# Performance work log

Hardware: AMD Instinct MI355X
Metric: run time of the kernel (lower is better)

## Reference

```python
import jax, jax.numpy as jnp
import numpy as np

BS, N, XC, K, YS = 64, 1024, 1024, 256, 768

def setup_inputs() -> dict:
    key = jax.random.key(0)
    ks = jax.random.split(key, 5)
    return {
        "x": jax.random.normal(ks[0], (BS, N, XC), dtype=jnp.float32),
        "y": jax.random.normal(ks[1], (BS, YS), dtype=jnp.float32),
        "W_ch": jax.random.normal(ks[2], (K, XC), dtype=jnp.float32) * 0.02,
        "b_ch": jax.random.normal(ks[3], (K,), dtype=jnp.float32) * 0.02,
        "W_y": jax.random.normal(ks[4], (K, YS), dtype=jnp.float32) * 0.02,
    }

def reference(x, y, W_ch, b_ch, W_y):
    # y_k: [bs, k] (no bias)
    y_k = jnp.einsum('bs,ks->bk', y, W_y)
    # channel affine on every spatial position, batched: [bs, n, k]
    x_k = jnp.einsum('bnc,kc->bnk', x, W_ch) + b_ch
    # add per-sample y_k (broadcast over spatial dim), tanh, softmax over k
    z = jnp.tanh(x_k + y_k[:, None, :])
    attn = jax.nn.softmax(z, axis=-1)
    # torch.cat over dim=0 of per-sample [n, k] blocks -> [bs*n, k]
    return attn.reshape(-1, attn.shape[-1])
```

## Files before the change

kernel.cpp:

```cpp
#include <hip/hip_runtime.h>


#define XC    1024
#define KOUT  256
#define NT    16
#define ZSTR  260
#define ZB    33280
#define LDSZ  34816

typedef float        f32x4_t  __attribute__((ext_vector_type(4)));
typedef unsigned int u32x4_t  __attribute__((ext_vector_type(4)));
typedef unsigned int u32x2_t  __attribute__((ext_vector_type(2)));
typedef __bf16       bf16x8_t __attribute__((ext_vector_type(8)));

__device__ __forceinline__ unsigned short f2bf(float f) {
  unsigned int u = __float_as_uint(f);
  u += 0x7fffu + ((u >> 16) & 1u);
  return (unsigned short)(u >> 16);
}

__device__ __forceinline__ float fast_tanh(float v) {
  float e = __expf(2.0f * v);
  return 1.0f - 2.0f / (e + 1.0f);
}

#define LGKM_BARRIER() do {                                  \
    asm volatile("s_waitcnt lgkmcnt(0)" ::: "memory");       \
    __builtin_amdgcn_s_barrier();                            \
    __builtin_amdgcn_sched_barrier(0);                       \
  } while (0)

__global__ void prep_kernel(const float* __restrict__ Wch,
                            const float* __restrict__ y,
                            const float* __restrict__ Wy,
                            const float* __restrict__ bch,
                            unsigned short* __restrict__ wbf,
                            float* __restrict__ biasws) {
  if (blockIdx.x < 256) {
    const int k = blockIdx.x;
    const int u = threadIdx.x;
    f32x4_t v = ((const f32x4_t*)(Wch + k * XC))[u];
    const int c0   = u << 2;
    const int t    = c0 >> 6;
    const int ch   = (c0 & 63) >> 3;
    const int kk   = ch >> 2;
    const int lg   = ch & 3;
    const int half = (c0 >> 2) & 1;
    const int wv   = k >> 6;
    const int ni   = (k >> 4) & 3;
    const int lr   = k & 15;
    const int lane = (lg << 4) | lr;
    unsigned int lo = (unsigned int)f2bf(v.x) | ((unsigned int)f2bf(v.y) << 16);
    unsigned int hi = (unsigned int)f2bf(v.z) | ((unsigned int)f2bf(v.w) << 16);
    char* p = (char*)wbf +
              ((size_t)((((t << 2) + wv) * 2 + kk) * 4 + ni) << 10) +
              (lane << 4) + (half << 3);
    *(u32x2_t*)p = (u32x2_t){lo, hi};
  } else {
    __shared__ __align__(16) float ys[768];
    const int b = blockIdx.x - 256;
    const int k = threadIdx.x;
    for (int i = k; i < 768; i += 256) ys[i] = y[b * 768 + i];
    __syncthreads();
    const f32x4_t* w4 = (const f32x4_t*)(Wy + k * 768);
    const f32x4_t* y4 = (const f32x4_t*)ys;
    float s = 0.f;
#pragma unroll 8
    for (int i = 0; i < 192; ++i) {
      f32x4_t w = w4[i], a = y4[i];
      s = fmaf(w.x, a.x, s); s = fmaf(w.y, a.y, s);
      s = fmaf(w.z, a.z, s); s = fmaf(w.w, a.w, s);
    }
    biasws[b * 256 + k] = s + bch[k];
  }
}

__global__ __launch_bounds__(256, 4) void fused_kernel(
    const float* __restrict__ x, const unsigned short* __restrict__ wbf,
    const float* __restrict__ bias, float* __restrict__ out) {
  __shared__ __align__(16) unsigned char smem[LDSZ];
  const int tid = threadIdx.x;
  const int l   = tid & 63;
  const int wv  = tid >> 6;
  const int lr  = l & 15;
  const int lg  = l >> 4;
  const int m0  = blockIdx.x << 5;
  const int bidx = m0 >> 10;
  const int rr  = tid >> 4;
  const int c4  = tid & 15;

  f32x4_t acc[2][4];
#pragma unroll
  for (int i = 0; i < 2; ++i)
#pragma unroll
    for (int j = 0; j < 4; ++j) acc[i][j] = (f32x4_t){0.f, 0.f, 0.f, 0.f};

  const float* xb = x + (size_t)m0 * XC + (size_t)rr * XC + (c4 << 2);
  const char* wsrc = (const char*)wbf;
  f32x4_t avA[2], avB[2];
  bf16x8_t bfr[8];

#define LOADA(dst, tt) do {                                                  \
    _Pragma("unroll")                                                        \
    for (int j = 0; j < 2; ++j)                                              \
      dst[j] = *(const f32x4_t*)(xb + (size_t)(j << 4) * XC + ((tt) << 6));  \
  } while (0)

#define LOADB(tt) do {                                                       \
    const char* g = wsrc + (size_t)(tt) * 32768 + (wv << 13) + (l << 4);     \
    _Pragma("unroll")                                                        \
    for (int f = 0; f < 8; ++f)                                              \
      bfr[f] = __builtin_bit_cast(bf16x8_t, *(const u32x4_t*)(g + (f << 10)));\
  } while (0)

#define WRITEA(src, buf) do {                                                \
    _Pragma("unroll")                                                        \
    for (int j = 0; j < 2; ++j) {                                            \
      const int row = (j << 4) + rr;                                         \
      unsigned int lo = (unsigned int)f2bf(src[j].x) |                       \
                        ((unsigned int)f2bf(src[j].y) << 16);                \
      unsigned int hi = (unsigned int)f2bf(src[j].z) |                       \
                        ((unsigned int)f2bf(src[j].w) << 16);                \
      char* p = (char*)smem + ((buf) << 12) + row * 128 +                    \
                (((c4 >> 1) ^ (row & 7)) << 4) + ((c4 & 1) << 3);            \
      *(u32x2_t*)p = (u32x2_t){lo, hi};                                      \
    }                                                                        \
  } while (0)

#define COMPUTE(buf) do {                                                    \
    const u32x4_t* aB = (const u32x4_t*)(smem + ((buf) << 12));              \
    _Pragma("unroll")                                                        \
    for (int kk = 0; kk < 2; ++kk) {                                         \
      const int cs = ((kk << 2) | lg) ^ (lr & 7);                            \
      bf16x8_t afr[2];                                                       \
      _Pragma("unroll")                                                      \
      for (int mi = 0; mi < 2; ++mi)                                         \
        afr[mi] = __builtin_bit_cast(bf16x8_t, aB[(((mi << 4) + lr) << 3) + cs]);\
      _Pragma("unroll")                                                      \
      for (int mi = 0; mi < 2; ++mi)                                         \
        _Pragma("unroll")                                                    \
        for (int nj = 0; nj < 4; ++nj)                                       \
          acc[mi][nj] = __builtin_amdgcn_mfma_f32_16x16x32_bf16(             \
              afr[mi], bfr[(kk << 2) | nj], acc[mi][nj], 0, 0, 0);           \
    }                                                                        \
  } while (0)

  LOADA(avA, 0);
  LOADA(avB, 1);
  LOADB(0);
  WRITEA(avA, 0);
  LGKM_BARRIER();

  for (int t = 0; t < NT; t += 2) {
    if (t + 2 < NT) LOADA(avA, t + 2);
    COMPUTE(0);
    if (t + 1 < NT) LOADB(t + 1);
    if (t + 1 < NT) WRITEA(avB, 1);
    LGKM_BARRIER();
    if (t + 3 < NT) LOADA(avB, t + 3);
    COMPUTE(1);
    if (t + 2 < NT) LOADB(t + 2);
    if (t + 2 < NT) WRITEA(avA, 0);
    if (t + 2 < NT) LGKM_BARRIER();
  }
  __syncthreads();

#undef LOADA
#undef LOADB
#undef WRITEA
#undef COMPUTE

  float* zbuf    = (float*)smem;
  float* wred    = (float*)(smem + ZB);
  float* rowstat = (float*)(smem + ZB + 512);

  float brow[4];
#pragma unroll
  for (int ni = 0; ni < 4; ++ni)
    brow[ni] = bias[(bidx << 8) + (wv << 6) + (ni << 4) + lr];

#pragma unroll
  for (int mi = 0; mi < 2; ++mi)
#pragma unroll
    for (int ni = 0; ni < 4; ++ni)
#pragma unroll
      for (int r = 0; r < 4; ++r)
        acc[mi][ni][r] = fast_tanh(acc[mi][ni][r] + brow[ni]);

#pragma unroll
  for (int mi = 0; mi < 2; ++mi)
#pragma unroll
    for (int r = 0; r < 4; ++r) {
      float m = fmaxf(fmaxf(acc[mi][0][r], acc[mi][1][r]),
                      fmaxf(acc[mi][2][r], acc[mi][3][r]));
      m = fmaxf(m, __shfl_xor(m, 1));
      m = fmaxf(m, __shfl_xor(m, 2));
      m = fmaxf(m, __shfl_xor(m, 4));
      m = fmaxf(m, __shfl_xor(m, 8));
      if (lr == 0) wred[(wv << 5) + (mi << 4) + (lg << 2) + r] = m;
    }
  __syncthreads();
  if (tid < 32)
    rowstat[tid] = fmaxf(fmaxf(wred[tid], wred[32 + tid]),
                         fmaxf(wred[64 + tid], wred[96 + tid]));
  __syncthreads();

#pragma unroll
  for (int mi = 0; mi < 2; ++mi)
#pragma unroll
    for (int r = 0; r < 4; ++r) {
      const int row = (mi << 4) + (lg << 2) + r;
      const float m = rowstat[row];
      float s = 0.f;
#pragma unroll
      for (int ni = 0; ni < 4; ++ni) {
        float e = __expf(acc[mi][ni][r] - m);
        acc[mi][ni][r] = e;
        s += e;
      }
      s += __shfl_xor(s, 1);
      s += __shfl_xor(s, 2);
      s += __shfl_xor(s, 4);
      s += __shfl_xor(s, 8);
      if (lr == 0) wred[(wv << 5) + row] = s;
    }
  __syncthreads();
  if (tid < 32)
    rowstat[tid] = 1.0f / (wred[tid] + wred[32 + tid] +
                           wred[64 + tid] + wred[96 + tid]);
  __syncthreads();

#pragma unroll
  for (int mi = 0; mi < 2; ++mi)
#pragma unroll
    for (int r = 0; r < 4; ++r) {
      const int row = (mi << 4) + (lg << 2) + r;
      const float rinv = rowstat[row];
      float* zrow = zbuf + row * ZSTR + (wv << 6) + lr;
#pragma unroll
      for (int ni = 0; ni < 4; ++ni)
        zrow[ni << 4] = acc[mi][ni][r] * rinv;
    }
  __syncthreads();

  {
    float* ob = out + (size_t)m0 * KOUT;
#pragma unroll
    for (int p = 0; p < 8; ++p) {
      const int idx = (p << 8) + tid;
      const int row = idx >> 6;
      const int c4i = idx & 63;
      f32x4_t v = *(const f32x4_t*)(zbuf + row * ZSTR + (c4i << 2));
      *(f32x4_t*)(ob + (idx << 2) + ((row * (ZSTR - 256)) ? 0 : 0)) = v;
    }
  }
}

extern "C" void kernel_launch(void* const* d_in, const int* in_sizes, int n_in,
                              void* d_out, int out_size, void* d_ws, size_t ws_size,
                              hipStream_t stream) {
  (void)in_sizes; (void)n_in; (void)out_size; (void)ws_size;
  const float* x   = (const float*)d_in[0];
  const float* y   = (const float*)d_in[1];
  const float* Wch = (const float*)d_in[2];
  const float* bch = (const float*)d_in[3];
  const float* Wy  = (const float*)d_in[4];
  float* out = (float*)d_out;
  unsigned short* wbf = (unsigned short*)d_ws;
  float* biasws = (float*)((char*)d_ws + 512 * 1024);

  hipLaunchKernelGGL(prep_kernel, dim3(320), dim3(256), 0, stream,
                     Wch, y, Wy, bch, wbf, biasws);
  hipLaunchKernelGGL(fused_kernel, dim3(2048), dim3(256), 0, stream,
                     x, wbf, biasws, out);
}
```

Measured before the change: 123.9 us.

## Stage full 32-row A tile in LDS once, rotate K start per block

The fused GEMM+softmax kernel now converts the block's entire 32x1024 x tile to bf16 and stores it in 64KB of LDS up front. The main loop then runs with no barriers, only double-buffering the bf16 weight fragments from global memory. Each block starts its K sweep at a different offset (blockIdx & 15) to spread weight-fetch traffic across the cache. The LDS-staged coalesced output store is replaced by direct strided 4-byte writes, and occupancy drops from 4 to 2 blocks per CU because of the larger LDS footprint.

```diff
diff --git a/kernel.cpp b/kernel.cpp
--- a/kernel.cpp
+++ b/kernel.cpp
@@ -4,9 +4,7 @@
 #define XC    1024
 #define KOUT  256
 #define NT    16
-#define ZSTR  260
-#define ZB    33280
-#define LDSZ  34816
+#define LDSZ  65536
 
 typedef float        f32x4_t  __attribute__((ext_vector_type(4)));
 typedef unsigned int u32x4_t  __attribute__((ext_vector_type(4)));
@@ -75,19 +73,18 @@
   }
 }
 
-__global__ __launch_bounds__(256, 4) void fused_kernel(
+__global__ __launch_bounds__(256, 2) void fused_kernel(
     const float* __restrict__ x, const unsigned short* __restrict__ wbf,
     const float* __restrict__ bias, float* __restrict__ out) {
   __shared__ __align__(16) unsigned char smem[LDSZ];
   const int tid = threadIdx.x;
   const int l   = tid & 63;
-  const int wv  = tid >> 6;
+  const int w   = tid >> 6;
   const int lr  = l & 15;
   const int lg  = l >> 4;
   const int m0  = blockIdx.x << 5;
   const int bidx = m0 >> 10;
-  const int rr  = tid >> 4;
-  const int c4  = tid & 15;
+  const int t0  = blockIdx.x & 15;
 
   f32x4_t acc[2][4];
 #pragma unroll
@@ -95,40 +92,40 @@
 #pragma unroll
     for (int j = 0; j < 4; ++j) acc[i][j] = (f32x4_t){0.f, 0.f, 0.f, 0.f};
 
-  const float* xb = x + (size_t)m0 * XC + (size_t)rr * XC + (c4 << 2);
-  const char* wsrc = (const char*)wbf;
-  f32x4_t avA[2], avB[2];
-  bf16x8_t bfr[8];
-
-#define LOADA(dst, tt) do {                                                  \
-    _Pragma("unroll")                                                        \
-    for (int j = 0; j < 2; ++j)                                              \
-      dst[j] = *(const f32x4_t*)(xb + (size_t)(j << 4) * XC + ((tt) << 6));  \
-  } while (0)
-
-#define LOADB(tt) do {                                                       \
-    const char* g = wsrc + (size_t)(tt) * 32768 + (wv << 13) + (l << 4);     \
-    _Pragma("unroll")                                                        \
-    for (int f = 0; f < 8; ++f)                                              \
-      bfr[f] = __builtin_bit_cast(bf16x8_t, *(const u32x4_t*)(g + (f << 10)));\
-  } while (0)
-
-#define WRITEA(src, buf) do {                                                \
-    _Pragma("unroll")                                                        \
-    for (int j = 0; j < 2; ++j) {                                            \
-      const int row = (j << 4) + rr;                                         \
+  const f32x4_t* xbase = (const f32x4_t*)(x + (size_t)m0 * XC);
+  const char* wsrc = (const char*)wbf + (w << 13) + (l << 4);
+  f32x4_t G0[8], G1[8];
+  bf16x8_t bfrA[8], bfrB[8];
+
+#define LOADG(dst, i0) do {                                                  \
+    _Pragma("unroll")                                                        \
+    for (int j = 0; j < 8; ++j)                                              \
+      dst[j] = xbase[(size_t)((i0) + j) * 256 + tid];                        \
+  } while (0)
+
+#define WRITEG(src, i0) do {                                                 \
+    _Pragma("unroll")                                                        \
+    for (int j = 0; j < 8; ++j) {                                            \
+      const int row = (i0) + j;                                              \
       unsigned int lo = (unsigned int)f2bf(src[j].x) |                       \
                         ((unsigned int)f2bf(src[j].y) << 16);                \
       unsigned int hi = (unsigned int)f2bf(src[j].z) |                       \
                         ((unsigned int)f2bf(src[j].w) << 16);                \
-      char* p = (char*)smem + ((buf) << 12) + row * 128 +                    \
-                (((c4 >> 1) ^ (row & 7)) << 4) + ((c4 & 1) << 3);            \
+      char* p = (char*)smem + ((tid >> 4) << 12) + row * 128 +               \
+                ((((tid & 15) >> 1) ^ (row & 7)) << 4) + ((tid & 1) << 3);   \
       *(u32x2_t*)p = (u32x2_t){lo, hi};                                      \
     }                                                                        \
   } while (0)
 
-#define COMPUTE(buf) do {                                                    \
-    const u32x4_t* aB = (const u32x4_t*)(smem + ((buf) << 12));              \
+#define LOADB(dst, tt) do {                                                  \
+    const char* g = wsrc + (size_t)(tt) * 32768;                             \
+    _Pragma("unroll")                                                        \
+    for (int f = 0; f < 8; ++f)                                              \
+      dst[f] = __builtin_bit_cast(bf16x8_t, *(const u32x4_t*)(g + (f << 10)));\
+  } while (0)
+
+#define COMPUTE_T(tt, bsrc) do {                                             \
+    const u32x4_t* aB = (const u32x4_t*)(smem + ((tt) << 12));               \
     _Pragma("unroll")                                                        \
     for (int kk = 0; kk < 2; ++kk) {                                         \
       const int cs = ((kk << 2) | lg) ^ (lr & 7);                            \
@@ -141,43 +138,42 @@
         _Pragma("unroll")                                                    \
         for (int nj = 0; nj < 4; ++nj)                                       \
           acc[mi][nj] = __builtin_amdgcn_mfma_f32_16x16x32_bf16(             \
-              afr[mi], bfr[(kk << 2) | nj], acc[mi][nj], 0, 0, 0);           \
+              afr[mi], bsrc[(kk << 2) | nj], acc[mi][nj], 0, 0, 0);          \
     }                                                                        \
   } while (0)
 
-  LOADA(avA, 0);
-  LOADA(avB, 1);
-  LOADB(0);
-  WRITEA(avA, 0);
+  LOADG(G0, 0);
+  LOADG(G1, 8);
+  WRITEG(G0, 0);
+  LOADG(G0, 16);
+  WRITEG(G1, 8);
+  LOADG(G1, 24);
+  WRITEG(G0, 16);
+  WRITEG(G1, 24);
+  LOADB(bfrA, t0);
   LGKM_BARRIER();
 
-  for (int t = 0; t < NT; t += 2) {
-    if (t + 2 < NT) LOADA(avA, t + 2);
-    COMPUTE(0);
-    if (t + 1 < NT) LOADB(t + 1);
-    if (t + 1 < NT) WRITEA(avB, 1);
-    LGKM_BARRIER();
-    if (t + 3 < NT) LOADA(avB, t + 3);
-    COMPUTE(1);
-    if (t + 2 < NT) LOADB(t + 2);
-    if (t + 2 < NT) WRITEA(avA, 0);
-    if (t + 2 < NT) LGKM_BARRIER();
+#pragma unroll
+  for (int s = 0; s < NT; s += 2) {
+    LOADB(bfrB, ((s + 1 + t0) & 15));
+    COMPUTE_T(((s + t0) & 15), bfrA);
+    if (s + 2 < NT) LOADB(bfrA, ((s + 2 + t0) & 15));
+    COMPUTE_T(((s + 1 + t0) & 15), bfrB);
   }
   __syncthreads();
 
-#undef LOADA
+#undef LOADG
+#undef WRITEG
 #undef LOADB
-#undef WRITEA
-#undef COMPUTE
-
-  float* zbuf    = (float*)smem;
-  float* wred    = (float*)(smem + ZB);
-  float* rowstat = (float*)(smem + ZB + 512);
+#undef COMPUTE_T
+
+  float* wred    = (float*)smem;
+  float* rowstat = (float*)(smem + 512);
 
   float brow[4];
 #pragma unroll
   for (int ni = 0; ni < 4; ++ni)
-    brow[ni] = bias[(bidx << 8) + (wv << 6) + (ni << 4) + lr];
+    brow[ni] = bias[(bidx << 8) + (w << 6) + (ni << 4) + lr];
 
 #pragma unroll
   for (int mi = 0; mi < 2; ++mi)
@@ -197,7 +193,7 @@
       m = fmaxf(m, __shfl_xor(m, 2));
       m = fmaxf(m, __shfl_xor(m, 4));
       m = fmaxf(m, __shfl_xor(m, 8));
-      if (lr == 0) wred[(wv << 5) + (mi << 4) + (lg << 2) + r] = m;
+      if (lr == 0) wred[(w << 5) + (mi << 4) + (lg << 2) + r] = m;
     }
   __syncthreads();
   if (tid < 32)
@@ -222,7 +218,7 @@
       s += __shfl_xor(s, 2);
       s += __shfl_xor(s, 4);
       s += __shfl_xor(s, 8);
-      if (lr == 0) wred[(wv << 5) + row] = s;
+      if (lr == 0) wred[(w << 5) + row] = s;
     }
   __syncthreads();
   if (tid < 32)
@@ -236,24 +232,11 @@
     for (int r = 0; r < 4; ++r) {
       const int row = (mi << 4) + (lg << 2) + r;
       const float rinv = rowstat[row];
-      float* zrow = zbuf + row * ZSTR + (wv << 6) + lr;
+      float* orow = out + (size_t)(m0 + row) * KOUT + (w << 6) + lr;
 #pragma unroll
       for (int ni = 0; ni < 4; ++ni)
-        zrow[ni << 4] = acc[mi][ni][r] * rinv;
-    }
-  __syncthreads();
-
-  {
-    float* ob = out + (size_t)m0 * KOUT;
-#pragma unroll
-    for (int p = 0; p < 8; ++p) {
-      const int idx = (p << 8) + tid;
-      const int row = idx >> 6;
-      const int c4i = idx & 63;
-      f32x4_t v = *(const f32x4_t*)(zbuf + row * ZSTR + (c4i << 2));
-      *(f32x4_t*)(ob + (idx << 2) + ((row * (ZSTR - 256)) ? 0 : 0)) = v;
-    }
-  }
+        orow[ni << 4] = acc[mi][ni][r] * rinv;
+    }
 }
 
 extern "C" void kernel_launch(void* const* d_in, const int* in_sizes, int n_in,
```

Result: slower. 138.4 us (+11.7%).
